# Kernel tuning notes

Measured on AMD Instinct MI355X. Metric: run time of the kernel, lower is better.

Reference implementation:

```python
import jax, jax.numpy as jnp
import numpy as np

N = 4096   # nodes
D = 512    # feature dim
E = 65536  # edges
HOPS = 10  # APPNP K (init arg 'hops')
ALPHA = 0.5


def setup_inputs() -> dict:
    key = jax.random.key(0)
    k1, k2, k3 = jax.random.split(key, 3)
    x_train = jax.random.normal(k1, (N, D), dtype=jnp.float32)
    # kernel_scale = nn.Linear(D, 1, bias=False) weight, flattened to [D]
    w = jax.random.normal(k2, (D,), dtype=jnp.float32) * 0.05
    edge_index = jax.random.randint(k3, (2, E), 0, N, dtype=jnp.int32)
    return {"x_train": x_train, "w": w, "edge_index": edge_index}


def appnp(x0, src, dst, hops, alpha):
    # torch_geometric APPNP with gcn_norm (add self-loops, symmetric norm), dropout=0
    n = x0.shape[0]
    loop = jnp.arange(n, dtype=src.dtype)
    s = jnp.concatenate([src, loop])
    d = jnp.concatenate([dst, loop])
    deg = jax.ops.segment_sum(jnp.ones_like(s, dtype=x0.dtype), d, num_segments=n)
    dis = deg ** -0.5  # deg >= 1 thanks to self-loops
    norm = dis[s] * dis[d]

    def body(h, _):
        agg = jax.ops.segment_sum(norm[:, None] * h[s], d, num_segments=n)
        return (1.0 - alpha) * agg + alpha * x0, None

    h, _ = jax.lax.scan(body, x0, None, length=hops)
    return h


def reference(x_train, w, edge_index):
    n = x_train.shape[0]
    # RBF_kernel: K[i,j] = sum_d w_d * (x_i - x_j)_d^2 for i != j, diag = 1 (the eye)
    xw = x_train * w                                   # [N, D]
    sq = jnp.sum(xw * x_train, axis=1)                 # [N] weighted squared norms
    K = sq[:, None] + sq[None, :] - 2.0 * (xw @ x_train.T)  # [N, N]
    idx = jnp.arange(n)
    K = K.at[idx, idx].set(1.0)

    src, dst = edge_index[0], edge_index[1]
    kgg = appnp(K, src, dst, HOPS, ALPHA)
    kgg = appnp(kgg.T, src, dst, HOPS, ALPHA)

    # adj = dense coo(edge_index, ones); diag = (diag(adj.sum(dim=1)) + 1) ** -0.5
    # (adds 1 to the WHOLE matrix, so off-diagonal entries become 1.0 -- faithful)
    deg_row = jax.ops.segment_sum(jnp.ones((edge_index.shape[1],), K.dtype), src, num_segments=n)
    Dmat = (jnp.diag(deg_row) + 1.0) ** -0.5           # [N, N]
    kgg = Dmat * kgg       # elementwise, as in the original
    kgg = Dmat * kgg.T
    return kgg
```

## Files before the change

kernel.cpp:

```cpp
#include <hip/hip_runtime.h>
#include <stdint.h>

#define Nn 4096
#define Dd 512
#define Ee 65536
#define HOPS 10
#define TPB 512
#define RPT (Nn / TPB)
#define CT 4
#define WCAP 64
#define BCOLS 516
#define KEXT 1536

typedef short bf16x8 __attribute__((ext_vector_type(8)));
typedef float f32x4 __attribute__((ext_vector_type(4)));

__device__ __forceinline__ unsigned short bf16r(float x) {
  unsigned int b = __float_as_uint(x);
  return (unsigned short)((b + 0x7FFFu + ((b >> 16) & 1u)) >> 16);
}
__device__ __forceinline__ float ubf(unsigned short h) {
  return __uint_as_float(((unsigned int)h) << 16);
}
__device__ __forceinline__ void gld16(const unsigned short* g, unsigned short* lds) {
  __builtin_amdgcn_global_load_lds(
      (const __attribute__((address_space(1))) unsigned int*)g,
      (__attribute__((address_space(3))) unsigned int*)lds, 16, 0, 0);
}

__global__ __launch_bounds__(256) void k_sq(const float* __restrict__ x,
                                            const float* __restrict__ w,
                                            float* __restrict__ sq) {
  int row = blockIdx.x;
  int tid = threadIdx.x;
  const float* xr = x + (size_t)row * Dd;
  float partial = 0.f;
  for (int d = tid; d < Dd; d += 256) {
    float xv = xr[d];
    partial += xv * xv * w[d];
  }
  for (int off = 32; off >= 1; off >>= 1) partial += __shfl_down(partial, off, 64);
  __shared__ float red[4];
  int wv = tid >> 6, ln = tid & 63;
  if (ln == 0) red[wv] = partial;
  __syncthreads();
  if (tid == 0) sq[row] = red[0] + red[1] + red[2] + red[3];
}

__global__ void k_count(const int* __restrict__ src, const int* __restrict__ dst,
                        int* __restrict__ degi, int* __restrict__ degrow) {
  int e = blockIdx.x * blockDim.x + threadIdx.x;
  if (e < Ee) {
    atomicAdd(&degi[dst[e]], 1);
    atomicAdd(&degrow[src[e]], 1);
  }
}

__global__ void k_dis(const int* __restrict__ degi, const int* __restrict__ degrow,
                      float* __restrict__ dis, float* __restrict__ d2) {
  int i = blockIdx.x * 256 + threadIdx.x;
  dis[i] = rsqrtf((float)(degi[i] + 1));
  d2[i] = 1.0f / ((float)degrow[i] + 1.0f);
}

__global__ void k_hist(const int* __restrict__ degi, int* __restrict__ binbase) {
  __shared__ int h[WCAP + 1];
  int t = threadIdx.x;
  if (t <= WCAP) h[t] = 0;
  __syncthreads();
  for (int i = t; i < Nn; i += 256) {
    int d = degi[i] + 1;
    if (d > WCAP) d = WCAP;
    atomicAdd(&h[d], 1);
  }
  __syncthreads();
  if (t == 0) {
    int run = 0;
    for (int b = 0; b <= WCAP; b++) { int c = h[b]; binbase[b] = run; run += c; }
  }
}

__global__ void k_scatter(const int* __restrict__ degi, const int* __restrict__ binbase,
                          int* __restrict__ bincnt, int* __restrict__ perm,
                          int* __restrict__ rnk) {
  int i = blockIdx.x * 256 + threadIdx.x;
  int d = degi[i] + 1;
  if (d > WCAP) d = WCAP;
  int pos = binbase[d] + atomicAdd(&bincnt[d], 1);
  perm[pos] = i;
  rnk[i] = pos;
}

__global__ void k_wsub(const int* __restrict__ degi, const int* __restrict__ perm,
                       int* __restrict__ wsub) {
  int t = threadIdx.x;
  int d = degi[perm[t * 64 + 63]] + 1;
  wsub[t] = d > WCAP ? WCAP : d;
}

__global__ void k_fill_ell(const int* __restrict__ src, const int* __restrict__ dst,
                           const float* __restrict__ dis, const int* __restrict__ rnk,
                           int* __restrict__ slot, int2* __restrict__ ell) {
  int i = blockIdx.x * blockDim.x + threadIdx.x;
  if (i < Ee) {
    int s = src[i], d = dst[i];
    int p = atomicAdd(&slot[d], 1);
    if (p < WCAP) ell[(size_t)p * Nn + rnk[d]] = make_int2(s, __float_as_int(dis[s] * dis[d]));
  } else if (i < Ee + Nn) {
    int v = i - Ee;
    int p = atomicAdd(&slot[v], 1);
    if (p < WCAP) ell[(size_t)p * Nn + rnk[v]] = make_int2(v, __float_as_int(dis[v] * dis[v]));
  }
}

__global__ __launch_bounds__(256) void k_xpose(const float* __restrict__ x,
                                               float* __restrict__ xcat) {
  __shared__ float tile[32][33];
  int cx = blockIdx.x, rx = blockIdx.y;
  int t = threadIdx.x, txc = t & 31, tyc = t >> 5;
#pragma unroll
  for (int i = 0; i < 4; i++) {
    int a = tyc + i * 8;
    tile[a][txc] = x[(size_t)(rx * 32 + a) * Dd + cx * 32 + txc];
  }
  __syncthreads();
#pragma unroll
  for (int i = 0; i < 4; i++) {
    int a = tyc + i * 8;
    int c = cx * 32 + a;
    xcat[(size_t)c * Nn + rx * 32 + txc] = tile[txc][a];
  }
}

__global__ void k_tail(const float* __restrict__ sq, float* __restrict__ xcat) {
  int r = blockIdx.x * 256 + threadIdx.x;
  xcat[(size_t)512 * Nn + r] = sq[r];
  xcat[(size_t)513 * Nn + r] = 1.0f;
  xcat[(size_t)514 * Nn + r] = 0.0f;
  xcat[(size_t)515 * Nn + r] = 0.0f;
}

template <int MODE>
__global__ __launch_bounds__(TPB, 4) void k_appnp(const float* __restrict__ xsrc,
                                                  const float* __restrict__ wp,
                                                  unsigned short* __restrict__ mb,
                                                  unsigned short* __restrict__ aext,
                                                  unsigned short* __restrict__ bext,
                                                  float* __restrict__ mu,
                                                  float* __restrict__ m1,
                                                  const int2* __restrict__ ell,
                                                  const int* __restrict__ perm,
                                                  const int* __restrict__ wsub) {
  extern __shared__ float4 h4[];
  int j0 = blockIdx.x * CT;
  int tid = threadIdx.x;
  int wv = tid >> 6, ln = tid & 63;
  int qb = wv * 512 + ln;

#pragma unroll
  for (int rr = 0; rr < RPT; rr++) {
    int r = tid + rr * TPB;
    float4 v;
    if (MODE == 1) {
      v.x = (r == j0 + 0) ? 1.f : 0.f;
      v.y = (r == j0 + 1) ? 1.f : 0.f;
      v.z = (r == j0 + 2) ? 1.f : 0.f;
      v.w = (r == j0 + 3) ? 1.f : 0.f;
    } else {
      v.x = xsrc[(size_t)(j0 + 0) * Nn + r];
      v.y = xsrc[(size_t)(j0 + 1) * Nn + r];
      v.z = xsrc[(size_t)(j0 + 2) * Nn + r];
      v.w = xsrc[(size_t)(j0 + 3) * Nn + r];
    }
    h4[r] = v;
  }

  int ws[RPT];
#pragma unroll
  for (int rr = 0; rr < RPT; rr++)
    ws[rr] = __builtin_amdgcn_readfirstlane(wsub[wv * 8 + rr]);
  const int Wv = ws[RPT - 1];

  int rp[RPT];
#pragma unroll
  for (int rr = 0; rr < RPT; rr++) rp[rr] = perm[qb + rr * 64];

  __syncthreads();
  float4 x0r[RPT];
#pragma unroll
  for (int rr = 0; rr < RPT; rr++) x0r[rr] = h4[rp[rr]];

  float4 acc[RPT];
  for (int it = 0; it < HOPS; it++) {
    int2 cur[RPT];
#pragma unroll
    for (int rr = 0; rr < RPT; rr++) cur[rr] = ell[qb + rr * 64];
#pragma unroll
    for (int rr = 0; rr < RPT; rr++) acc[rr] = x0r[rr];
    for (int s = 0; s < Wv; s++) {
      int sn = s + 1;
      int2 nxt[RPT];
#pragma unroll
      for (int rr = 0; rr < RPT; rr++)
        if (sn < ws[rr]) nxt[rr] = ell[(size_t)sn * Nn + qb + rr * 64];
#pragma unroll
      for (int rr = 0; rr < RPT; rr++)
        if (s < ws[rr]) {
          float vv = __int_as_float(cur[rr].y);
          float4 hu = h4[cur[rr].x];
          acc[rr].x = fmaf(vv, hu.x, acc[rr].x);
          acc[rr].y = fmaf(vv, hu.y, acc[rr].y);
          acc[rr].z = fmaf(vv, hu.z, acc[rr].z);
          acc[rr].w = fmaf(vv, hu.w, acc[rr].w);
        }
#pragma unroll
      for (int rr = 0; rr < RPT; rr++)
        if (sn < ws[rr]) cur[rr] = nxt[rr];
    }
#pragma unroll
    for (int rr = 0; rr < RPT; rr++) {
      acc[rr].x *= 0.5f; acc[rr].y *= 0.5f; acc[rr].z *= 0.5f; acc[rr].w *= 0.5f;
    }
    __syncthreads();
#pragma unroll
    for (int rr = 0; rr < RPT; rr++) h4[rp[rr]] = acc[rr];
    __syncthreads();
  }

  if (MODE == 1) {
#pragma unroll
    for (int rr = 0; rr < RPT; rr++) {
      int r = tid + rr * TPB;
      float4 a = h4[r];
      ushort4 o = make_ushort4(bf16r(a.x), bf16r(a.y), bf16r(a.z), bf16r(a.w));
      *(ushort4*)&mb[(size_t)r * Nn + j0] = o;
    }
  } else {
    if (j0 < 512) {
      float w0 = -2.f * wp[j0 + 0], w1 = -2.f * wp[j0 + 1];
      float w2 = -2.f * wp[j0 + 2], w3 = -2.f * wp[j0 + 3];
#pragma unroll
      for (int rr = 0; rr < RPT; rr++) {
        int r = tid + rr * TPB;
        float4 a = h4[r];
        ushort4 yhi = make_ushort4(bf16r(a.x), bf16r(a.y), bf16r(a.z), bf16r(a.w));
        ushort4 ylo = make_ushort4(bf16r(a.x - ubf(yhi.x)), bf16r(a.y - ubf(yhi.y)),
                                   bf16r(a.z - ubf(yhi.z)), bf16r(a.w - ubf(yhi.w)));
        float4 p = make_float4(w0 * a.x, w1 * a.y, w2 * a.z, w3 * a.w);
        ushort4 phi = make_ushort4(bf16r(p.x), bf16r(p.y), bf16r(p.z), bf16r(p.w));
        ushort4 plo = make_ushort4(bf16r(p.x - ubf(phi.x)), bf16r(p.y - ubf(phi.y)),
                                   bf16r(p.z - ubf(phi.z)), bf16r(p.w - ubf(phi.w)));
        *(ushort4*)&bext[(size_t)r * KEXT + j0] = yhi;
        *(ushort4*)&bext[(size_t)r * KEXT + 512 + j0] = ylo;
        *(ushort4*)&bext[(size_t)r * KEXT + 1024 + j0] = yhi;
        *(ushort4*)&aext[(size_t)r * KEXT + j0] = phi;
        *(ushort4*)&aext[(size_t)r * KEXT + 512 + j0] = phi;
        *(ushort4*)&aext[(size_t)r * KEXT + 1024 + j0] = plo;
      }
    } else if (j0 == 512) {
#pragma unroll
      for (int rr = 0; rr < RPT; rr++) {
        int r = tid + rr * TPB;
        float4 a = h4[r];
        mu[r] = a.x;
        m1[r] = a.y;
      }
    }
  }
}

__device__ __forceinline__ void mm_step(const unsigned short* __restrict__ Ap, int lda,
                                        const unsigned short* __restrict__ Bp, int ldb,
                                        unsigned short* As, unsigned short* Bs,
                                        int i0, int j0, int k0, int l, int w, int wr,
                                        int wc, f32x4 acc[4][4]) {
  int rsub = w * 8 + (l >> 3);
  int scg = ((l & 7) ^ (l >> 3)) * 8;
#pragma unroll
  for (int r = 0; r < 4; r++) {
    int row = r * 32 + rsub;
    gld16(Ap + (size_t)(i0 + row) * lda + k0 + scg, As + (r * 32 + w * 8) * 64);
    gld16(Bp + (size_t)(j0 + row) * ldb + k0 + scg, Bs + (r * 32 + w * 8) * 64);
  }
  __syncthreads();
#pragma unroll
  for (int q = 0; q < 2; q++) {
    bf16x8 af[4], bg[4];
#pragma unroll
    for (int m = 0; m < 4; m++) {
      int ar = wr * 64 + m * 16 + (l & 15);
      af[m] = *(const bf16x8*)(As + ar * 64 + ((((l >> 4) + 4 * q) ^ (ar & 7)) * 8));
      int br = wc * 64 + m * 16 + (l & 15);
      bg[m] = *(const bf16x8*)(Bs + br * 64 + ((((l >> 4) + 4 * q) ^ (br & 7)) * 8));
    }
#pragma unroll
    for (int m = 0; m < 4; m++)
#pragma unroll
      for (int n = 0; n < 4; n++)
        acc[m][n] = __builtin_amdgcn_mfma_f32_16x16x32_bf16(af[m], bg[n], acc[m][n], 0, 0, 0);
  }
  __syncthreads();
}

__global__ __launch_bounds__(256) void k_mm(const unsigned short* __restrict__ Mb,
                                            const unsigned short* __restrict__ Aext,
                                            const unsigned short* __restrict__ Bext,
                                            const float* __restrict__ mu,
                                            const float* __restrict__ m1,
                                            const float* __restrict__ d2,
                                            float* __restrict__ out) {
  __shared__ unsigned short As[128 * 64];
  __shared__ unsigned short Bs[128 * 64];
  int lid = blockIdx.y * 32 + blockIdx.x;
  int swz = (lid & 7) * 128 + (lid >> 3);
  int i0 = (swz >> 5) * 128, j0 = (swz & 31) * 128;
  int tid = threadIdx.x, l = tid & 63, w = tid >> 6;
  int wr = w >> 1, wc = w & 1;
  f32x4 acc[4][4];
#pragma unroll
  for (int m = 0; m < 4; m++)
#pragma unroll
    for (int n = 0; n < 4; n++) acc[m][n] = (f32x4){0.f, 0.f, 0.f, 0.f};

  for (int k0 = 0; k0 < Nn; k0 += 64)
    mm_step(Mb, Nn, Mb, Nn, As, Bs, i0, j0, k0, l, w, wr, wc, acc);
  for (int k0 = 0; k0 < KEXT; k0 += 64)
    mm_step(Aext, KEXT, Bext, KEXT, As, Bs, i0, j0, k0, l, w, wr, wc, acc);

#pragma unroll
  for (int m = 0; m < 4; m++) {
#pragma unroll
    for (int n = 0; n < 4; n++) {
#pragma unroll
      for (int q = 0; q < 4; q++) {
        int gi = i0 + wr * 64 + m * 16 + ((l >> 4) << 2) + q;
        int gj = j0 + wc * 64 + n * 16 + (l & 15);
        float v = acc[m][n][q] + mu[gi] * m1[gj] + m1[gi] * mu[gj];
        if (gi == gj) v *= d2[gi];
        out[(size_t)gi * Nn + gj] = v;
      }
    }
  }
}

extern "C" void kernel_launch(void* const* d_in, const int* in_sizes, int n_in,
                              void* d_out, int out_size, void* d_ws, size_t ws_size,
                              hipStream_t stream) {
  const float* x = (const float*)d_in[0];
  const float* w = (const float*)d_in[1];
  const int* ei = (const int*)d_in[2];
  const int* src = ei;
  const int* dstv = ei + Ee;
  float* out = (float*)d_out;

  unsigned short* Mb = (unsigned short*)d_ws;
  float* xcat = (float*)d_ws;
  unsigned short* aext = (unsigned short*)((char*)d_ws + (size_t)Nn * Nn * 2);
  unsigned short* bext = aext + (size_t)Nn * KEXT;
  int2* ell = (int2*)(bext + (size_t)Nn * KEXT);
  float* sq = (float*)(ell + (size_t)WCAP * Nn);
  float* dis = sq + Nn;
  float* d2 = dis + Nn;
  float* mu = d2 + Nn;
  float* m1 = mu + Nn;
  int* degi = (int*)(m1 + Nn);
  int* degrow = degi + Nn;
  int* slotcnt = degrow + Nn;
  int* bincnt = slotcnt + Nn;
  int* binbase = bincnt + (WCAP + 1);
  int* perm = binbase + (WCAP + 1);
  int* rnk = perm + Nn;
  int* wsub = rnk + Nn;

  hipMemsetAsync(ell, 0, (size_t)WCAP * Nn * sizeof(int2), stream);
  hipMemsetAsync(degi, 0, sizeof(int) * (3 * Nn + (WCAP + 1)), stream);

  k_sq<<<Nn, 256, 0, stream>>>(x, w, sq);
  k_count<<<Ee / 256, 256, 0, stream>>>(src, dstv, degi, degrow);
  k_dis<<<Nn / 256, 256, 0, stream>>>(degi, degrow, dis, d2);
  k_hist<<<1, 256, 0, stream>>>(degi, binbase);
  k_scatter<<<Nn / 256, 256, 0, stream>>>(degi, binbase, bincnt, perm, rnk);
  k_wsub<<<1, 64, 0, stream>>>(degi, perm, wsub);
  k_fill_ell<<<(Ee + Nn + 255) / 256, 256, 0, stream>>>(src, dstv, dis, rnk, slotcnt, ell);
  k_xpose<<<dim3(16, 128), 256, 0, stream>>>(x, xcat);
  k_tail<<<Nn / 256, 256, 0, stream>>>(sq, xcat);

  k_appnp<0><<<BCOLS / CT, TPB, Nn * sizeof(float4), stream>>>(xcat, w, nullptr, aext, bext,
                                                               mu, m1, ell, perm, wsub);
  k_appnp<1><<<Nn / CT, TPB, Nn * sizeof(float4), stream>>>(nullptr, nullptr, Mb, nullptr,
                                                            nullptr, nullptr, nullptr, ell,
                                                            perm, wsub);
  k_mm<<<dim3(32, 32), 256, 0, stream>>>(Mb, aext, bext, mu, m1, d2, out);
}
```

Measured before the change: 971.7 us.

## Replace sparse propagation of feature columns with dense GEMM against propagation matrix

Rather than running the APPNP sparse propagation a second time over the 516 feature/extra columns, the code now reuses the dense propagation matrix M (computed from identity columns) and forms Y = M·X with a new MFMA GEMM kernel. X is stored as a hi/lo bf16 split so the product keeps near-fp32 accuracy. The GEMM epilogue then builds the extended A/B operands plus the mu and m1 vectors. This removes one 129-block sparse-propagation launch and adds a 4096x640x8192 bf16 GEMM. The propagation matrix itself is stored only in bf16, so Y may lose some accuracy compared with propagating X directly in fp32.

```diff
diff --git a/kernel.cpp b/kernel.cpp
--- a/kernel.cpp
+++ b/kernel.cpp
@@ -9,8 +9,9 @@
 #define RPT (Nn / TPB)
 #define CT 4
 #define WCAP 64
-#define BCOLS 516
 #define KEXT 1536
+#define YC 640
+#define XK 8192
 
 typedef short bf16x8 __attribute__((ext_vector_type(8)));
 typedef float f32x4 __attribute__((ext_vector_type(4)));
@@ -114,7 +115,7 @@
 }
 
 __global__ __launch_bounds__(256) void k_xpose(const float* __restrict__ x,
-                                               float* __restrict__ xcat) {
+                                               unsigned short* __restrict__ xb) {
   __shared__ float tile[32][33];
   int cx = blockIdx.x, rx = blockIdx.y;
   int t = threadIdx.x, txc = t & 31, tyc = t >> 5;
@@ -128,26 +129,24 @@
   for (int i = 0; i < 4; i++) {
     int a = tyc + i * 8;
     int c = cx * 32 + a;
-    xcat[(size_t)c * Nn + rx * 32 + txc] = tile[txc][a];
-  }
-}
-
-__global__ void k_tail(const float* __restrict__ sq, float* __restrict__ xcat) {
+    float v = tile[txc][a];
+    unsigned short hi = bf16r(v);
+    xb[(size_t)c * XK + rx * 32 + txc] = hi;
+    xb[(size_t)c * XK + Nn + rx * 32 + txc] = bf16r(v - ubf(hi));
+  }
+}
+
+__global__ void k_tail(const float* __restrict__ sq, unsigned short* __restrict__ xb) {
   int r = blockIdx.x * 256 + threadIdx.x;
-  xcat[(size_t)512 * Nn + r] = sq[r];
-  xcat[(size_t)513 * Nn + r] = 1.0f;
-  xcat[(size_t)514 * Nn + r] = 0.0f;
-  xcat[(size_t)515 * Nn + r] = 0.0f;
-}
-
-template <int MODE>
-__global__ __launch_bounds__(TPB, 4) void k_appnp(const float* __restrict__ xsrc,
-                                                  const float* __restrict__ wp,
-                                                  unsigned short* __restrict__ mb,
-                                                  unsigned short* __restrict__ aext,
-                                                  unsigned short* __restrict__ bext,
-                                                  float* __restrict__ mu,
-                                                  float* __restrict__ m1,
+  float v = sq[r];
+  unsigned short hi = bf16r(v);
+  xb[(size_t)512 * XK + r] = hi;
+  xb[(size_t)512 * XK + Nn + r] = bf16r(v - ubf(hi));
+  xb[(size_t)513 * XK + r] = bf16r(1.0f);
+  xb[(size_t)513 * XK + Nn + r] = 0;
+}
+
+__global__ __launch_bounds__(TPB, 4) void k_appnp(unsigned short* __restrict__ mb,
                                                   const int2* __restrict__ ell,
                                                   const int* __restrict__ perm,
                                                   const int* __restrict__ wsub) {
@@ -161,17 +160,10 @@
   for (int rr = 0; rr < RPT; rr++) {
     int r = tid + rr * TPB;
     float4 v;
-    if (MODE == 1) {
-      v.x = (r == j0 + 0) ? 1.f : 0.f;
-      v.y = (r == j0 + 1) ? 1.f : 0.f;
-      v.z = (r == j0 + 2) ? 1.f : 0.f;
-      v.w = (r == j0 + 3) ? 1.f : 0.f;
-    } else {
-      v.x = xsrc[(size_t)(j0 + 0) * Nn + r];
-      v.y = xsrc[(size_t)(j0 + 1) * Nn + r];
-      v.z = xsrc[(size_t)(j0 + 2) * Nn + r];
-      v.w = xsrc[(size_t)(j0 + 3) * Nn + r];
-    }
+    v.x = (r == j0 + 0) ? 1.f : 0.f;
+    v.y = (r == j0 + 1) ? 1.f : 0.f;
+    v.z = (r == j0 + 2) ? 1.f : 0.f;
+    v.w = (r == j0 + 3) ? 1.f : 0.f;
     h4[r] = v;
   }
 
@@ -227,45 +219,12 @@
     __syncthreads();
   }
 
-  if (MODE == 1) {
-#pragma unroll
-    for (int rr = 0; rr < RPT; rr++) {
-      int r = tid + rr * TPB;
-      float4 a = h4[r];
-      ushort4 o = make_ushort4(bf16r(a.x), bf16r(a.y), bf16r(a.z), bf16r(a.w));
-      *(ushort4*)&mb[(size_t)r * Nn + j0] = o;
-    }
-  } else {
-    if (j0 < 512) {
-      float w0 = -2.f * wp[j0 + 0], w1 = -2.f * wp[j0 + 1];
-      float w2 = -2.f * wp[j0 + 2], w3 = -2.f * wp[j0 + 3];
-#pragma unroll
-      for (int rr = 0; rr < RPT; rr++) {
-        int r = tid + rr * TPB;
-        float4 a = h4[r];
-        ushort4 yhi = make_ushort4(bf16r(a.x), bf16r(a.y), bf16r(a.z), bf16r(a.w));
-        ushort4 ylo = make_ushort4(bf16r(a.x - ubf(yhi.x)), bf16r(a.y - ubf(yhi.y)),
-                                   bf16r(a.z - ubf(yhi.z)), bf16r(a.w - ubf(yhi.w)));
-        float4 p = make_float4(w0 * a.x, w1 * a.y, w2 * a.z, w3 * a.w);
-        ushort4 phi = make_ushort4(bf16r(p.x), bf16r(p.y), bf16r(p.z), bf16r(p.w));
-        ushort4 plo = make_ushort4(bf16r(p.x - ubf(phi.x)), bf16r(p.y - ubf(phi.y)),
-                                   bf16r(p.z - ubf(phi.z)), bf16r(p.w - ubf(phi.w)));
-        *(ushort4*)&bext[(size_t)r * KEXT + j0] = yhi;
-        *(ushort4*)&bext[(size_t)r * KEXT + 512 + j0] = ylo;
-        *(ushort4*)&bext[(size_t)r * KEXT + 1024 + j0] = yhi;
-        *(ushort4*)&aext[(size_t)r * KEXT + j0] = phi;
-        *(ushort4*)&aext[(size_t)r * KEXT + 512 + j0] = phi;
-        *(ushort4*)&aext[(size_t)r * KEXT + 1024 + j0] = plo;
-      }
-    } else if (j0 == 512) {
-#pragma unroll
-      for (int rr = 0; rr < RPT; rr++) {
-        int r = tid + rr * TPB;
-        float4 a = h4[r];
-        mu[r] = a.x;
-        m1[r] = a.y;
-      }
-    }
+#pragma unroll
+  for (int rr = 0; rr < RPT; rr++) {
+    int r = tid + rr * TPB;
+    float4 a = h4[r];
+    ushort4 o = make_ushort4(bf16r(a.x), bf16r(a.y), bf16r(a.z), bf16r(a.w));
+    *(ushort4*)&mb[(size_t)r * Nn + j0] = o;
   }
 }
 
@@ -300,6 +259,60 @@
         acc[m][n] = __builtin_amdgcn_mfma_f32_16x16x32_bf16(af[m], bg[n], acc[m][n], 0, 0, 0);
   }
   __syncthreads();
+}
+
+__global__ __launch_bounds__(256) void k_ymm(const unsigned short* __restrict__ Mb,
+                                             const unsigned short* __restrict__ xb,
+                                             const float* __restrict__ wp,
+                                             unsigned short* __restrict__ aext,
+                                             unsigned short* __restrict__ bext,
+                                             float* __restrict__ mu,
+                                             float* __restrict__ m1) {
+  __shared__ unsigned short As[128 * 64];
+  __shared__ unsigned short Bs[128 * 64];
+  int i0 = blockIdx.y * 128, j0 = blockIdx.x * 128;
+  int tid = threadIdx.x, l = tid & 63, w = tid >> 6;
+  int wr = w >> 1, wc = w & 1;
+  f32x4 acc[4][4];
+#pragma unroll
+  for (int m = 0; m < 4; m++)
+#pragma unroll
+    for (int n = 0; n < 4; n++) acc[m][n] = (f32x4){0.f, 0.f, 0.f, 0.f};
+
+  for (int k0 = 0; k0 < Nn; k0 += 64)
+    mm_step(Mb, Nn, xb, XK, As, Bs, i0, j0, k0, l, w, wr, wc, acc);
+  for (int k0 = 0; k0 < Nn; k0 += 64)
+    mm_step(Mb, Nn, xb + Nn, XK, As, Bs, i0, j0, k0, l, w, wr, wc, acc);
+
+#pragma unroll
+  for (int m = 0; m < 4; m++) {
+#pragma unroll
+    for (int n = 0; n < 4; n++) {
+#pragma unroll
+      for (int q = 0; q < 4; q++) {
+        int gi = i0 + wr * 64 + m * 16 + ((l >> 4) << 2) + q;
+        int gj = j0 + wc * 64 + n * 16 + (l & 15);
+        float y = acc[m][n][q];
+        if (gj < 512) {
+          unsigned short yhi = bf16r(y);
+          unsigned short ylo = bf16r(y - ubf(yhi));
+          float p = -2.f * wp[gj] * y;
+          unsigned short phi = bf16r(p);
+          unsigned short plo = bf16r(p - ubf(phi));
+          bext[(size_t)gi * KEXT + gj] = yhi;
+          bext[(size_t)gi * KEXT + 512 + gj] = ylo;
+          bext[(size_t)gi * KEXT + 1024 + gj] = yhi;
+          aext[(size_t)gi * KEXT + gj] = phi;
+          aext[(size_t)gi * KEXT + 512 + gj] = phi;
+          aext[(size_t)gi * KEXT + 1024 + gj] = plo;
+        } else if (gj == 512) {
+          mu[gi] = y;
+        } else if (gj == 513) {
+          m1[gi] = y;
+        }
+      }
+    }
+  }
 }
 
 __global__ __launch_bounds__(256) void k_mm(const unsigned short* __restrict__ Mb,
@@ -354,10 +367,10 @@
   float* out = (float*)d_out;
 
   unsigned short* Mb = (unsigned short*)d_ws;
-  float* xcat = (float*)d_ws;
-  unsigned short* aext = (unsigned short*)((char*)d_ws + (size_t)Nn * Nn * 2);
+  unsigned short* aext = Mb + (size_t)Nn * Nn;
   unsigned short* bext = aext + (size_t)Nn * KEXT;
-  int2* ell = (int2*)(bext + (size_t)Nn * KEXT);
+  unsigned short* xb = bext + (size_t)Nn * KEXT;
+  int2* ell = (int2*)(xb + (size_t)YC * XK);
   float* sq = (float*)(ell + (size_t)WCAP * Nn);
   float* dis = sq + Nn;
   float* d2 = dis + Nn;
@@ -374,6 +387,7 @@
 
   hipMemsetAsync(ell, 0, (size_t)WCAP * Nn * sizeof(int2), stream);
   hipMemsetAsync(degi, 0, sizeof(int) * (3 * Nn + (WCAP + 1)), stream);
+  hipMemsetAsync(xb, 0, (size_t)YC * XK * sizeof(unsigned short), stream);
 
   k_sq<<<Nn, 256, 0, stream>>>(x, w, sq);
   k_count<<<Ee / 256, 256, 0, stream>>>(src, dstv, degi, degrow);
@@ -382,13 +396,10 @@
   k_scatter<<<Nn / 256, 256, 0, stream>>>(degi, binbase, bincnt, perm, rnk);
   k_wsub<<<1, 64, 0, stream>>>(degi, perm, wsub);
   k_fill_ell<<<(Ee + Nn + 255) / 256, 256, 0, stream>>>(src, dstv, dis, rnk, slotcnt, ell);
-  k_xpose<<<dim3(16, 128), 256, 0, stream>>>(x, xcat);
-  k_tail<<<Nn / 256, 256, 0, stream>>>(sq, xcat);
-
-  k_appnp<0><<<BCOLS / CT, TPB, Nn * sizeof(float4), stream>>>(xcat, w, nullptr, aext, bext,
-                                                               mu, m1, ell, perm, wsub);
-  k_appnp<1><<<Nn / CT, TPB, Nn * sizeof(float4), stream>>>(nullptr, nullptr, Mb, nullptr,
-                                                            nullptr, nullptr, nullptr, ell,
-                                                            perm, wsub);
+  k_xpose<<<dim3(16, 128), 256, 0, stream>>>(x, xb);
+  k_tail<<<Nn / 256, 256, 0, stream>>>(sq, xb);
+
+  k_appnp<<<Nn / CT, TPB, Nn * sizeof(float4), stream>>>(Mb, ell, perm, wsub);
+  k_ymm<<<dim3(YC / 128, Nn / 128), 256, 0, stream>>>(Mb, xb, w, aext, bext, mu, m1);
   k_mm<<<dim3(32, 32), 256, 0, stream>>>(Mb, aext, bext, mu, m1, d2, out);
 }
```

Result: faster. 908.3 us (-6.5%).
